# Kernel optimization log

Measured on AMD Instinct MI355X. Metric: run time of the kernel, lower is better.

## Reference

```python
import jax, jax.numpy as jnp
import numpy as np

B, S, E, H = 4, 2048, 1024, 16
HD = E // H  # per-head dim = 64


def setup_inputs() -> dict:
    key = jax.random.key(0)
    ks = jax.random.split(key, 12)
    scale = 1.0 / np.sqrt(E)
    inp = {
        "q": jax.random.normal(ks[0], (B, S, E), jnp.float32),
        "k": jax.random.normal(ks[1], (B, S, E), jnp.float32),
        "v": jax.random.normal(ks[2], (B, S, E), jnp.float32),
        # causal mask: True = masked out (matches torch masked_fill_ semantics)
        "mask": jnp.triu(jnp.ones((S, S), jnp.bool_), k=1)[None, None, :, :],
        "Wq": jax.random.normal(ks[3], (E, E), jnp.float32) * scale,
        "bq": jnp.zeros((E,), jnp.float32),
        "Wk": jax.random.normal(ks[4], (E, E), jnp.float32) * scale,
        "bk": jnp.zeros((E,), jnp.float32),
        "Wv": jax.random.normal(ks[5], (E, E), jnp.float32) * scale,
        "bv": jnp.zeros((E,), jnp.float32),
        "Wo": jax.random.normal(ks[6], (E, E), jnp.float32) * scale,
        "bo": jnp.zeros((E,), jnp.float32),
    }
    return inp


def reference(q, k, v, mask, Wq, bq, Wk, bk, Wv, bv, Wo, bo):
    # QKV projections (nn.Linear: x @ W.T + b)
    query = q @ Wq.T + bq
    key_ = k @ Wk.T + bk
    value = v @ Wv.T + bv
    # split heads: [B, S, E] -> [B, H, S, HD]
    mq = query.reshape(B, S, H, HD).transpose(0, 2, 1, 3)
    mk = key_.reshape(B, S, H, HD).transpose(0, 2, 1, 3)
    mv = value.reshape(B, S, H, HD).transpose(0, 2, 1, 3)
    # scaled dot-product attention with explicit score matrix [B, H, S, S]
    scores = jnp.einsum("bhqd,bhkd->bhqk", mq, mk) / jnp.sqrt(jnp.float32(HD))
    scores = jnp.where(mask, -jnp.inf, scores)
    probs = jax.nn.softmax(scores, axis=-1)
    ctx = jnp.einsum("bhqk,bhkd->bhqd", probs, mv)
    # merge heads and output projection
    ctx = ctx.transpose(0, 2, 1, 3).reshape(B, S, E)
    return ctx @ Wo.T + bo
```

## Files before the change

kernel.cpp:

```cpp
#include <hip/hip_runtime.h>
#include <hip/hip_bf16.h>
#include <math.h>

#define B_ 4
#define S_ 2048
#define E_ 1024
#define H_ 16
#define HD_ 64
#define NEG_ (-1e30f)
#define SC2_ 0.18033688f
#define EXP2(x) __builtin_amdgcn_exp2f(x)

typedef __bf16 bf16x8 __attribute__((ext_vector_type(8)));
typedef float f32x4 __attribute__((ext_vector_type(4)));

#define MFMA(a, b, c) __builtin_amdgcn_mfma_f32_16x16x32_bf16((a), (b), (c), 0, 0, 0)

#define GLDS16(gp, lp)                                                        \
  __builtin_amdgcn_global_load_lds(                                           \
      (const __attribute__((address_space(1))) void*)(gp),                    \
      (__attribute__((address_space(3))) void*)(lp), 16, 0, 0)

__device__ __forceinline__ bf16x8 cvt8(const float4 a, const float4 b) {
  bf16x8 r;
  r[0] = (__bf16)a.x; r[1] = (__bf16)a.y; r[2] = (__bf16)a.z; r[3] = (__bf16)a.w;
  r[4] = (__bf16)b.x; r[5] = (__bf16)b.y; r[6] = (__bf16)b.z; r[7] = (__bf16)b.w;
  return r;
}

__global__ __launch_bounds__(256)
void cvt_w_kernel(const float* __restrict__ wq, const float* __restrict__ wk,
                  const float* __restrict__ wv, const float* __restrict__ wo,
                  __bf16* __restrict__ wqb, __bf16* __restrict__ wkb,
                  __bf16* __restrict__ wvb, __bf16* __restrict__ wob)
{
  const int y = blockIdx.y;
  const float* src = (y == 0) ? wq : (y == 1) ? wk : (y == 2) ? wv : wo;
  __bf16* dst      = (y == 0) ? wqb: (y == 1) ? wkb: (y == 2) ? wvb: wob;
  const size_t i = ((size_t)blockIdx.x * 256 + threadIdx.x) * 8;
  const float4 a = *(const float4*)&src[i];
  const float4 b = *(const float4*)&src[i + 4];
  *(bf16x8*)&dst[i] = cvt8(a, b);
}

__global__ __launch_bounds__(256)
void cvt_in_kernel(const float* __restrict__ src, __bf16* __restrict__ dst)
{
  const size_t i = ((size_t)blockIdx.x * 256 + threadIdx.x) * 8;
  const float4 a = *(const float4*)&src[i];
  const float4 b = *(const float4*)&src[i + 4];
  *(bf16x8*)&dst[i] = cvt8(a, b);
}

__global__ __launch_bounds__(256, 3)
void qkv_gemm(const __bf16* __restrict__ Aq, const __bf16* __restrict__ Ak,
              const __bf16* __restrict__ Av,
              const __bf16* __restrict__ Wqb, const __bf16* __restrict__ Wkb,
              const __bf16* __restrict__ Wvb,
              const float* __restrict__ bq, const float* __restrict__ bk,
              const float* __restrict__ bv,
              __bf16* __restrict__ Qo, __bf16* __restrict__ Ko,
              __bf16* __restrict__ Vo, int zbase)
{
  __shared__ __align__(16) __bf16 sA[128 * 64];
  __shared__ __align__(16) __bf16 sB[128 * 64];
  const int z = (int)blockIdx.z + zbase;
  const __bf16* A   = (z == 0) ? Aq  : (z == 1) ? Ak  : Av;
  const __bf16* W   = (z == 0) ? Wqb : (z == 1) ? Wkb : Wvb;
  const float* bias = (z == 0) ? bq  : (z == 1) ? bk  : bv;
  __bf16* outp      = (z == 0) ? Qo  : (z == 1) ? Ko  : Vo;

  const int t = threadIdx.x;
  const int lane = t & 63, ln = lane & 15, qd = lane >> 4;
  const int l7 = ln & 7;
  const int wv_ = t >> 6, wm = (wv_ >> 1) * 64, wn = (wv_ & 1) * 64;
  const int m0 = ((int)blockIdx.x * 8 + ((int)blockIdx.y >> 3)) * 128;
  const int n0 = ((int)blockIdx.y & 7) * 128;

  f32x4 acc[4][4] = {};
  for (int kk = 0; kk < E_; kk += 64) {
    __syncthreads();
    for (int p = 0; p < 4; ++p) {
      const int c = t + 256 * p;
      const int row = c >> 3, kc = c & 7;
      const int gcol = ((kc ^ (row & 7)) * 8);
      GLDS16(A + (size_t)(m0 + row) * E_ + kk + gcol, sA + c * 8);
      GLDS16(W + (size_t)(n0 + row) * E_ + kk + gcol, sB + c * 8);
    }
    __syncthreads();
    for (int kb2 = 0; kb2 < 2; ++kb2) {
      const int sw = ((kb2 * 4 + qd) ^ l7) * 8;
      bf16x8 af[4], bf_[4];
      for (int i = 0; i < 4; ++i)
        af[i]  = *(const bf16x8*)&sA[(wm + i * 16 + ln) * 64 + sw];
      for (int j = 0; j < 4; ++j)
        bf_[j] = *(const bf16x8*)&sB[(wn + j * 16 + ln) * 64 + sw];
      for (int i = 0; i < 4; ++i)
        for (int j = 0; j < 4; ++j)
          acc[i][j] = MFMA(af[i], bf_[j], acc[i][j]);
    }
  }

  for (int j = 0; j < 4; ++j) {
    const int n = n0 + wn + j * 16 + ln;
    const float bb = bias[n];
    const int hh = n >> 6, d = n & 63;
    for (int i = 0; i < 4; ++i) {
      for (int r2 = 0; r2 < 4; ++r2) {
        const int m = m0 + wm + i * 16 + qd * 4 + r2;
        const int b = m >> 11, s2 = m & 2047;
        float val = acc[i][j][r2] + bb;
        if (z == 0) {
          val *= SC2_;
          ((__bf16*)outp)[((size_t)(b * H_ + hh) * S_ + s2) * HD_ + d] = (__bf16)val;
        } else if (z == 1) {
          ((__bf16*)outp)[((size_t)(b * H_ + hh) * S_ + s2) * HD_ + d] = (__bf16)val;
        } else {
          ((__bf16*)outp)[((size_t)(b * H_ + hh) * HD_ + d) * S_ + s2] = (__bf16)val;
        }
      }
    }
  }
}

__global__ __launch_bounds__(256, 3)
void attn_kernel(const __bf16* __restrict__ Qg, const __bf16* __restrict__ Kg,
                 const __bf16* __restrict__ Vg, __bf16* __restrict__ Og)
{
  const int slice = blockIdx.x;
  const int h = slice & 15, b = slice >> 4;
  const int qx = 31 - (int)blockIdx.y;
  const int t = threadIdx.x;
  const int wq = t >> 6;
  const int lane = t & 63;
  const int ln = lane & 15, qd = lane >> 4;
  const int l7 = ln & 7;
  const int q0 = qx * 64;
  const size_t bh = (size_t)(b * H_ + h);

  __shared__ __align__(16) __bf16 sK[128 * 64];
  __shared__ __align__(16) __bf16 sVt[64 * 128];
  __shared__ __align__(16) __bf16 sP[64 * 136];

  bf16x8 aq[2];
  {
    const __bf16* qrowp = Qg + (bh * S_ + q0 + wq * 16 + ln) * HD_;
    aq[0] = *(const bf16x8*)&qrowp[qd * 8];
    aq[1] = *(const bf16x8*)&qrowp[32 + qd * 8];
  }

  f32x4 o[4] = {};
  float m_prev[4], l_run[4];
  for (int r2 = 0; r2 < 4; ++r2) { m_prev[r2] = NEG_; l_run[r2] = 0.f; }

  const int ktmax = (q0 + 63) >> 7;
  for (int kt = 0; kt <= ktmax; ++kt) {
    const int k0 = kt * 128;
    __syncthreads();
    {
      const __bf16* kbase = Kg + (bh * S_ + k0) * HD_;
      const __bf16* vbase = Vg + bh * HD_ * S_ + k0;
      for (int p = 0; p < 4; ++p) {
        const int c = t + 256 * p;
        const int kr = c >> 3, kkc = c & 7;
        GLDS16(kbase + (size_t)kr * HD_ + ((kkc ^ (kr & 7)) * 8), sK + c * 8);
        const int vr = c >> 4, vkc = c & 15;
        GLDS16(vbase + (size_t)vr * S_ + ((vkc ^ (vr & 15)) * 8), sVt + c * 8);
      }
    }
    __syncthreads();

    f32x4 sc[8] = {};
    for (int kb2 = 0; kb2 < 2; ++kb2) {
      const int sw = ((kb2 * 4 + qd) ^ l7) * 8;
      for (int nt = 0; nt < 8; ++nt) {
        bf16x8 bk8 = *(const bf16x8*)&sK[(nt * 16 + ln) * 64 + sw];
        sc[nt] = MFMA(aq[kb2], bk8, sc[nt]);
      }
    }

    const int qrow = q0 + wq * 16 + qd * 4;
    float m_cur[4] = {NEG_, NEG_, NEG_, NEG_};
    if (k0 + 127 > q0) {
      for (int nt = 0; nt < 8; ++nt) {
        const int kcol = k0 + nt * 16 + ln;
        for (int r2 = 0; r2 < 4; ++r2) {
          float vv = sc[nt][r2];
          if (kcol > qrow + r2) vv = NEG_;
          sc[nt][r2] = vv;
          m_cur[r2] = fmaxf(m_cur[r2], vv);
        }
      }
    } else {
      for (int nt = 0; nt < 8; ++nt)
        for (int r2 = 0; r2 < 4; ++r2)
          m_cur[r2] = fmaxf(m_cur[r2], sc[nt][r2]);
    }
    for (int r2 = 0; r2 < 4; ++r2) {
      float vmx = m_cur[r2];
      for (int off = 1; off < 16; off <<= 1)
        vmx = fmaxf(vmx, __shfl_xor(vmx, off, 64));
      m_cur[r2] = vmx;
    }

    float alpha[4], rsum[4];
    for (int r2 = 0; r2 < 4; ++r2) {
      const float m_new = fmaxf(m_prev[r2], m_cur[r2]);
      alpha[r2] = EXP2(m_prev[r2] - m_new);
      m_prev[r2] = m_new;
      rsum[r2] = 0.f;
    }

    {
      const int rbase = (wq * 16 + qd * 4) * 136;
      for (int nt = 0; nt < 8; ++nt) {
        const int pcol = nt * 16 + ln;
        for (int r2 = 0; r2 < 4; ++r2) {
          const float p = EXP2(sc[nt][r2] - m_prev[r2]);
          rsum[r2] += p;
          sP[rbase + r2 * 136 + pcol] = (__bf16)p;
        }
      }
    }
    for (int r2 = 0; r2 < 4; ++r2) {
      float vs = rsum[r2];
      for (int off = 1; off < 16; off <<= 1)
        vs += __shfl_xor(vs, off, 64);
      l_run[r2] = l_run[r2] * alpha[r2] + vs;
    }
    for (int dt = 0; dt < 4; ++dt)
      for (int r2 = 0; r2 < 4; ++r2)
        o[dt][r2] *= alpha[r2];

    for (int ks = 0; ks < 4; ++ks) {
      bf16x8 ap = *(const bf16x8*)&sP[(wq * 16 + ln) * 136 + ks * 32 + qd * 8];
      const int swv = ((ks * 4 + qd) ^ ln) * 8;
      for (int dt = 0; dt < 4; ++dt) {
        bf16x8 bv8 = *(const bf16x8*)&sVt[(dt * 16 + ln) * 128 + swv];
        o[dt] = MFMA(ap, bv8, o[dt]);
      }
    }
  }

  for (int r2 = 0; r2 < 4; ++r2) {
    const int qrow = q0 + wq * 16 + qd * 4 + r2;
    const float inv = 1.0f / l_run[r2];
    for (int dt = 0; dt < 4; ++dt) {
      const int d = dt * 16 + ln;
      Og[((size_t)(b * S_ + qrow)) * E_ + h * HD_ + d] = (__bf16)(o[dt][r2] * inv);
    }
  }
}

__global__ __launch_bounds__(256, 3)
void out_gemm(const __bf16* __restrict__ A, const __bf16* __restrict__ W,
              const float* __restrict__ bias, float* __restrict__ out)
{
  __shared__ __align__(16) __bf16 sA[128 * 64];
  __shared__ __align__(16) __bf16 sB[128 * 64];
  const int t = threadIdx.x;
  const int lane = t & 63, ln = lane & 15, qd = lane >> 4;
  const int l7 = ln & 7;
  const int wv_ = t >> 6, wm = (wv_ >> 1) * 64, wn = (wv_ & 1) * 64;
  const int m0 = blockIdx.y * 128, n0 = blockIdx.x * 128;

  f32x4 acc[4][4] = {};
  for (int kk = 0; kk < E_; kk += 64) {
    __syncthreads();
    for (int p = 0; p < 4; ++p) {
      const int c = t + 256 * p;
      const int row = c >> 3, kc = c & 7;
      const int gcol = ((kc ^ (row & 7)) * 8);
      GLDS16(A + (size_t)(m0 + row) * E_ + kk + gcol, sA + c * 8);
      GLDS16(W + (size_t)(n0 + row) * E_ + kk + gcol, sB + c * 8);
    }
    __syncthreads();
    for (int kb2 = 0; kb2 < 2; ++kb2) {
      const int sw = ((kb2 * 4 + qd) ^ l7) * 8;
      bf16x8 af[4], bf_[4];
      for (int i = 0; i < 4; ++i)
        af[i]  = *(const bf16x8*)&sA[(wm + i * 16 + ln) * 64 + sw];
      for (int j = 0; j < 4; ++j)
        bf_[j] = *(const bf16x8*)&sB[(wn + j * 16 + ln) * 64 + sw];
      for (int i = 0; i < 4; ++i)
        for (int j = 0; j < 4; ++j)
          acc[i][j] = MFMA(af[i], bf_[j], acc[i][j]);
    }
  }

  for (int j = 0; j < 4; ++j) {
    const int n = n0 + wn + j * 16 + ln;
    const float bb = bias[n];
    for (int i = 0; i < 4; ++i)
      for (int r2 = 0; r2 < 4; ++r2) {
        const int m = m0 + wm + i * 16 + qd * 4 + r2;
        out[(size_t)m * E_ + n] = acc[i][j][r2] + bb;
      }
  }
}

extern "C" void kernel_launch(void* const* d_in, const int* in_sizes, int n_in,
                              void* d_out, int out_size, void* d_ws, size_t ws_size,
                              hipStream_t stream)
{
  const float* q  = (const float*)d_in[0];
  const float* k  = (const float*)d_in[1];
  const float* v  = (const float*)d_in[2];
  const float* Wq = (const float*)d_in[4];
  const float* bq = (const float*)d_in[5];
  const float* Wk = (const float*)d_in[6];
  const float* bk = (const float*)d_in[7];
  const float* Wv = (const float*)d_in[8];
  const float* bv = (const float*)d_in[9];
  const float* Wo = (const float*)d_in[10];
  const float* bo = (const float*)d_in[11];
  float* out = (float*)d_out;

  const size_t NE = (size_t)B_ * S_ * E_;
  const size_t NW = (size_t)E_ * E_;
  __bf16* Wqb = (__bf16*)d_ws;
  __bf16* Wkb = Wqb + NW;
  __bf16* Wvb = Wkb + NW;
  __bf16* Wob = Wvb + NW;
  __bf16* Qb  = Wob + NW;
  __bf16* Kb  = Qb + NE;
  __bf16* Vb  = Kb + NE;

  dim3 blk(256);
  cvt_w_kernel<<<dim3(512, 4), blk, 0, stream>>>(Wq, Wk, Wv, Wo,
                                                 Wqb, Wkb, Wvb, Wob);

  const size_t need_fat = (4 * NW + 6 * NE) * sizeof(__bf16);
  if (ws_size >= need_fat) {
    __bf16* q16 = Vb + NE;
    __bf16* k16 = q16 + NE;
    __bf16* v16 = k16 + NE;
    __bf16* Cb  = q16;
    cvt_in_kernel<<<dim3(4096), blk, 0, stream>>>(q, q16);
    cvt_in_kernel<<<dim3(4096), blk, 0, stream>>>(k, k16);
    cvt_in_kernel<<<dim3(4096), blk, 0, stream>>>(v, v16);
    qkv_gemm<<<dim3(8, 64, 3), blk, 0, stream>>>(q16, k16, v16,
                                                 Wqb, Wkb, Wvb,
                                                 bq, bk, bv, Qb, Kb, Vb, 0);
    attn_kernel<<<dim3(64, 32), blk, 0, stream>>>(Qb, Kb, Vb, Cb);
    out_gemm<<<dim3(8, 64), blk, 0, stream>>>(Cb, Wob, bo, out);
  } else {
    __bf16* X16 = Vb + NE;
    __bf16* Cb  = X16;
    const float* srcs[3] = {q, k, v};
    for (int z = 0; z < 3; ++z) {
      cvt_in_kernel<<<dim3(4096), blk, 0, stream>>>(srcs[z], X16);
      qkv_gemm<<<dim3(8, 64, 1), blk, 0, stream>>>(X16, X16, X16,
                                                   Wqb, Wkb, Wvb,
                                                   bq, bk, bv, Qb, Kb, Vb, z);
    }
    attn_kernel<<<dim3(64, 32), blk, 0, stream>>>(Qb, Kb, Vb, Cb);
    out_gemm<<<dim3(8, 64), blk, 0, stream>>>(Cb, Wob, bo, out);
  }
}
```

Before: 375.2 us.

## Transpose QK^T in attention and merge fp32-to-bf16 conversion kernels

The score MFMA now takes swapped operands, so each lane holds one query row (ln) across four keys. Row max and row sum then need only two cross-lane shuffles instead of four 4-step reductions, and P is written to LDS as packed 4-element bf16 vectors. Alpha and the final inverse are redistributed with __shfl to match the O accumulator layout. Separately, the four input and weight conversion launches are merged into one kernel to cut launch overhead. The packed 8-byte sP stores may bring LDS bank conflicts.

After: 332.8 us. 11.3% less time.

```diff
diff --git a/kernel.cpp b/kernel.cpp
--- a/kernel.cpp
+++ b/kernel.cpp
@@ -12,6 +12,7 @@
 #define EXP2(x) __builtin_amdgcn_exp2f(x)
 
 typedef __bf16 bf16x8 __attribute__((ext_vector_type(8)));
+typedef __bf16 bf16x4 __attribute__((ext_vector_type(4)));
 typedef float f32x4 __attribute__((ext_vector_type(4)));
 
 #define MFMA(a, b, c) __builtin_amdgcn_mfma_f32_16x16x32_bf16((a), (b), (c), 0, 0, 0)
@@ -26,6 +27,43 @@
   r[0] = (__bf16)a.x; r[1] = (__bf16)a.y; r[2] = (__bf16)a.z; r[3] = (__bf16)a.w;
   r[4] = (__bf16)b.x; r[5] = (__bf16)b.y; r[6] = (__bf16)b.z; r[7] = (__bf16)b.w;
   return r;
+}
+
+__device__ __forceinline__ f32x4 vmax4(f32x4 a, f32x4 b) {
+  f32x4 r;
+  r[0] = fmaxf(a[0], b[0]); r[1] = fmaxf(a[1], b[1]);
+  r[2] = fmaxf(a[2], b[2]); r[3] = fmaxf(a[3], b[3]);
+  return r;
+}
+
+__global__ __launch_bounds__(256)
+void cvt_all_kernel(const float* __restrict__ q, const float* __restrict__ k,
+                    const float* __restrict__ v,
+                    const float* __restrict__ wq, const float* __restrict__ wk,
+                    const float* __restrict__ wv, const float* __restrict__ wo,
+                    __bf16* __restrict__ q16, __bf16* __restrict__ k16,
+                    __bf16* __restrict__ v16,
+                    __bf16* __restrict__ wqb, __bf16* __restrict__ wkb,
+                    __bf16* __restrict__ wvb, __bf16* __restrict__ wob)
+{
+  const int bx = blockIdx.x;
+  const float* src;
+  __bf16* dst;
+  size_t off;
+  if (bx < 12288) {
+    const int z = bx >> 12, r = bx & 4095;
+    src = (z == 0) ? q : (z == 1) ? k : v;
+    dst = (z == 0) ? q16 : (z == 1) ? k16 : v16;
+    off = (size_t)r * 2048 + threadIdx.x * 8;
+  } else {
+    const int z = (bx - 12288) >> 9, r = (bx - 12288) & 511;
+    src = (z == 0) ? wq : (z == 1) ? wk : (z == 2) ? wv : wo;
+    dst = (z == 0) ? wqb : (z == 1) ? wkb : (z == 2) ? wvb : wob;
+    off = (size_t)r * 2048 + threadIdx.x * 8;
+  }
+  const float4 a = *(const float4*)&src[off];
+  const float4 b = *(const float4*)&src[off + 4];
+  *(bf16x8*)&dst[off] = cvt8(a, b);
 }
 
 __global__ __launch_bounds__(256)
@@ -149,9 +187,10 @@
     aq[1] = *(const bf16x8*)&qrowp[32 + qd * 8];
   }
 
+  const int myq = q0 + wq * 16 + ln;
+
   f32x4 o[4] = {};
-  float m_prev[4], l_run[4];
-  for (int r2 = 0; r2 < 4; ++r2) { m_prev[r2] = NEG_; l_run[r2] = 0.f; }
+  float m_prev = NEG_, l_run = 0.f;
 
   const int ktmax = (q0 + 63) >> 7;
   for (int kt = 0; kt <= ktmax; ++kt) {
@@ -174,63 +213,53 @@
     for (int kb2 = 0; kb2 < 2; ++kb2) {
       const int sw = ((kb2 * 4 + qd) ^ l7) * 8;
       for (int nt = 0; nt < 8; ++nt) {
-        bf16x8 bk8 = *(const bf16x8*)&sK[(nt * 16 + ln) * 64 + sw];
-        sc[nt] = MFMA(aq[kb2], bk8, sc[nt]);
-      }
-    }
-
-    const int qrow = q0 + wq * 16 + qd * 4;
-    float m_cur[4] = {NEG_, NEG_, NEG_, NEG_};
+        bf16x8 ak8 = *(const bf16x8*)&sK[(nt * 16 + ln) * 64 + sw];
+        sc[nt] = MFMA(ak8, aq[kb2], sc[nt]);
+      }
+    }
+
     if (k0 + 127 > q0) {
-      for (int nt = 0; nt < 8; ++nt) {
-        const int kcol = k0 + nt * 16 + ln;
-        for (int r2 = 0; r2 < 4; ++r2) {
-          float vv = sc[nt][r2];
-          if (kcol > qrow + r2) vv = NEG_;
-          sc[nt][r2] = vv;
-          m_cur[r2] = fmaxf(m_cur[r2], vv);
-        }
-      }
-    } else {
+      const int kb = k0 + qd * 4 - myq;
       for (int nt = 0; nt < 8; ++nt)
         for (int r2 = 0; r2 < 4; ++r2)
-          m_cur[r2] = fmaxf(m_cur[r2], sc[nt][r2]);
-    }
-    for (int r2 = 0; r2 < 4; ++r2) {
-      float vmx = m_cur[r2];
-      for (int off = 1; off < 16; off <<= 1)
-        vmx = fmaxf(vmx, __shfl_xor(vmx, off, 64));
-      m_cur[r2] = vmx;
-    }
-
-    float alpha[4], rsum[4];
-    for (int r2 = 0; r2 < 4; ++r2) {
-      const float m_new = fmaxf(m_prev[r2], m_cur[r2]);
-      alpha[r2] = EXP2(m_prev[r2] - m_new);
-      m_prev[r2] = m_new;
-      rsum[r2] = 0.f;
-    }
-
+          if (kb + nt * 16 + r2 > 0) sc[nt][r2] = NEG_;
+    }
+
+    f32x4 t0 = vmax4(vmax4(sc[0], sc[1]), vmax4(sc[2], sc[3]));
+    f32x4 t1 = vmax4(vmax4(sc[4], sc[5]), vmax4(sc[6], sc[7]));
+    f32x4 t2 = vmax4(t0, t1);
+    float mloc = fmaxf(fmaxf(t2[0], t2[1]), fmaxf(t2[2], t2[3]));
+    mloc = fmaxf(mloc, __shfl_xor(mloc, 16, 64));
+    mloc = fmaxf(mloc, __shfl_xor(mloc, 32, 64));
+    const float m_new = fmaxf(m_prev, mloc);
+    const float alpha = EXP2(m_prev - m_new);
+    m_prev = m_new;
+
+    float rsum = 0.f;
     {
-      const int rbase = (wq * 16 + qd * 4) * 136;
+      const int pb = (wq * 16 + ln) * 136 + qd * 4;
       for (int nt = 0; nt < 8; ++nt) {
-        const int pcol = nt * 16 + ln;
-        for (int r2 = 0; r2 < 4; ++r2) {
-          const float p = EXP2(sc[nt][r2] - m_prev[r2]);
-          rsum[r2] += p;
-          sP[rbase + r2 * 136 + pcol] = (__bf16)p;
-        }
-      }
-    }
-    for (int r2 = 0; r2 < 4; ++r2) {
-      float vs = rsum[r2];
-      for (int off = 1; off < 16; off <<= 1)
-        vs += __shfl_xor(vs, off, 64);
-      l_run[r2] = l_run[r2] * alpha[r2] + vs;
-    }
+        const float p0 = EXP2(sc[nt][0] - m_new);
+        const float p1 = EXP2(sc[nt][1] - m_new);
+        const float p2 = EXP2(sc[nt][2] - m_new);
+        const float p3 = EXP2(sc[nt][3] - m_new);
+        rsum += (p0 + p1) + (p2 + p3);
+        bf16x4 pk;
+        pk[0] = (__bf16)p0; pk[1] = (__bf16)p1;
+        pk[2] = (__bf16)p2; pk[3] = (__bf16)p3;
+        *(bf16x4*)&sP[pb + nt * 16] = pk;
+      }
+    }
+    rsum += __shfl_xor(rsum, 16, 64);
+    rsum += __shfl_xor(rsum, 32, 64);
+    l_run = l_run * alpha + rsum;
+
+    float af[4];
+    for (int r2 = 0; r2 < 4; ++r2)
+      af[r2] = __shfl(alpha, qd * 4 + r2, 64);
     for (int dt = 0; dt < 4; ++dt)
       for (int r2 = 0; r2 < 4; ++r2)
-        o[dt][r2] *= alpha[r2];
+        o[dt][r2] *= af[r2];
 
     for (int ks = 0; ks < 4; ++ks) {
       bf16x8 ap = *(const bf16x8*)&sP[(wq * 16 + ln) * 136 + ks * 32 + qd * 8];
@@ -242,12 +271,15 @@
     }
   }
 
+  const float linv = 1.0f / l_run;
+  float inv[4];
+  for (int r2 = 0; r2 < 4; ++r2)
+    inv[r2] = __shfl(linv, qd * 4 + r2, 64);
   for (int r2 = 0; r2 < 4; ++r2) {
     const int qrow = q0 + wq * 16 + qd * 4 + r2;
-    const float inv = 1.0f / l_run[r2];
     for (int dt = 0; dt < 4; ++dt) {
       const int d = dt * 16 + ln;
-      Og[((size_t)(b * S_ + qrow)) * E_ + h * HD_ + d] = (__bf16)(o[dt][r2] * inv);
+      Og[((size_t)(b * S_ + qrow)) * E_ + h * HD_ + d] = (__bf16)(o[dt][r2] * inv[r2]);
     }
   }
 }
@@ -327,24 +359,23 @@
   __bf16* Vb  = Kb + NE;
 
   dim3 blk(256);
-  cvt_w_kernel<<<dim3(512, 4), blk, 0, stream>>>(Wq, Wk, Wv, Wo,
-                                                 Wqb, Wkb, Wvb, Wob);
-
   const size_t need_fat = (4 * NW + 6 * NE) * sizeof(__bf16);
   if (ws_size >= need_fat) {
     __bf16* q16 = Vb + NE;
     __bf16* k16 = q16 + NE;
     __bf16* v16 = k16 + NE;
     __bf16* Cb  = q16;
-    cvt_in_kernel<<<dim3(4096), blk, 0, stream>>>(q, q16);
-    cvt_in_kernel<<<dim3(4096), blk, 0, stream>>>(k, k16);
-    cvt_in_kernel<<<dim3(4096), blk, 0, stream>>>(v, v16);
+    cvt_all_kernel<<<dim3(14336), blk, 0, stream>>>(q, k, v, Wq, Wk, Wv, Wo,
+                                                    q16, k16, v16,
+                                                    Wqb, Wkb, Wvb, Wob);
     qkv_gemm<<<dim3(8, 64, 3), blk, 0, stream>>>(q16, k16, v16,
                                                  Wqb, Wkb, Wvb,
                                                  bq, bk, bv, Qb, Kb, Vb, 0);
     attn_kernel<<<dim3(64, 32), blk, 0, stream>>>(Qb, Kb, Vb, Cb);
     out_gemm<<<dim3(8, 64), blk, 0, stream>>>(Cb, Wob, bo, out);
   } else {
+    cvt_w_kernel<<<dim3(512, 4), blk, 0, stream>>>(Wq, Wk, Wv, Wo,
+                                                   Wqb, Wkb, Wvb, Wob);
     __bf16* X16 = Vb + NE;
     __bf16* Cb  = X16;
     const float* srcs[3] = {q, k, v};
```
